# Performance work log

Measured on AMD Instinct MI355X. Metric: run time of the kernel, lower is better.

The kernel has to match this reference:

```python
import jax, jax.numpy as jnp
import numpy as np


def setup_inputs() -> dict:
    key = jax.random.key(0)
    k1, k2, k3, k4 = jax.random.split(key, 4)
    B, T, S, D = 256, 16, 32, 768
    return {
        "video_global": jax.random.normal(k1, (B, D), dtype=jnp.float32),
        "text_global": jax.random.normal(k2, (B, D), dtype=jnp.float32),
        "video_local": jax.random.normal(k3, (B, T, D), dtype=jnp.float32),
        "text_local": jax.random.normal(k4, (B, S, D), dtype=jnp.float32),
        "temp": jnp.zeros((1,), dtype=jnp.float32),  # log(1.0)
    }


def reference(video_global, text_global, video_local, text_local, temp):
    B = video_global.shape[0]
    logit_scale = jnp.exp(temp)[0]

    # ---- global contrastive loss ----
    global_sim = logit_scale * (video_global @ text_global.T)  # [B, B]
    diag = jnp.arange(B)
    loss_v2t = -jax.nn.log_softmax(global_sim, axis=1)[diag, diag].mean()
    loss_t2v = -jax.nn.log_softmax(global_sim, axis=0)[diag, diag].mean()
    loss_global = 0.5 * (loss_v2t + loss_t2v)

    # ---- local positive scores ----
    # paired (diagonal) local similarity: [B, T, S]
    sim_pos = logit_scale * jnp.einsum("btd,bsd->bts", video_local, text_local)
    time_weights = jax.nn.softmax(sim_pos.max(axis=-1), axis=-1)  # [B, T]
    pos_scores = (sim_pos.mean(axis=-1) * time_weights).sum(axis=1)  # [B]

    # ---- local negative scores (batched pairwise contraction) ----
    # [B, B, T, S]: video i vs text j, replacing the B*(B-1) tiny einsum loop
    sim_all = logit_scale * jnp.einsum("btd,csd->bcts", video_local, text_local)
    neg_full = (time_weights[:, None, :] * sim_all.mean(axis=-1)).sum(axis=-1)  # [B, B]

    # drop diagonal (i == j), preserving row-major loop order
    rows, cols = np.nonzero(~np.eye(B, dtype=bool))
    neg_scores = neg_full[rows, cols].reshape(B, B - 1)

    logits = jnp.concatenate([pos_scores[:, None], neg_scores], axis=-1)  # [B, B]
    loss_local = -jax.nn.log_softmax(logits, axis=-1)[:, 0].mean()

    return 0.6 * loss_global + 0.4 * loss_local
```

## Files before the change

### kernel.cpp

```cpp
#include <hip/hip_runtime.h>
#include <cmath>

#define BB 256
#define TT 16
#define SS 32
#define DD 768
#define LROW 260

__global__ __launch_bounds__(512) void hl_stage1(
    const float* __restrict__ vl, const float* __restrict__ tl,
    const float* __restrict__ temp,
    float* __restrict__ vw_ws, float* __restrict__ tb_ws)
{
    __shared__ float smem[12480];
    __shared__ float simb[512];
    __shared__ float rmax[16];
    __shared__ float twb[16];

    const int i   = blockIdx.x;
    const int tid = threadIdx.x;
    const float lsc = expf(temp[0]);

    const int slice = tid & 15;
    const int g     = tid >> 4;
    const int tg    = g >> 3;
    const int sg    = g & 7;

    const float* vli = vl + (size_t)i * TT * DD;
    const float* tli = tl + (size_t)i * SS * DD;

    float acc[4][4];
#pragma unroll
    for (int a = 0; a < 4; ++a)
#pragma unroll
        for (int b = 0; b < 4; ++b) acc[a][b] = 0.f;

    for (int c = 0; c < 3; ++c) {
        const int d0 = c << 8;
#pragma unroll
        for (int k = 0; k < 2; ++k) {
            int f4 = tid + (k << 9);
            int r  = f4 >> 6;
            int dc = (f4 & 63) << 2;
            *(float4*)&smem[r * LROW + dc] = *(const float4*)&vli[r * DD + d0 + dc];
        }
#pragma unroll
        for (int k = 0; k < 4; ++k) {
            int f4 = tid + (k << 9);
            int r  = f4 >> 6;
            int dc = (f4 & 63) << 2;
            *(float4*)&smem[(16 + r) * LROW + dc] = *(const float4*)&tli[r * DD + d0 + dc];
        }
        __syncthreads();
#pragma unroll
        for (int step = 0; step < 4; ++step) {
            const int db = (slice << 4) + (step << 2);
            float4 av[4], bv[4];
#pragma unroll
            for (int ti = 0; ti < 4; ++ti)
                av[ti] = *(const float4*)&smem[(tg * 4 + ti) * LROW + db];
#pragma unroll
            for (int sj = 0; sj < 4; ++sj)
                bv[sj] = *(const float4*)&smem[(16 + sg * 4 + sj) * LROW + db];
#pragma unroll
            for (int ti = 0; ti < 4; ++ti)
#pragma unroll
                for (int sj = 0; sj < 4; ++sj)
                    acc[ti][sj] += av[ti].x * bv[sj].x + av[ti].y * bv[sj].y
                                 + av[ti].z * bv[sj].z + av[ti].w * bv[sj].w;
        }
        __syncthreads();
    }

#pragma unroll
    for (int ti = 0; ti < 4; ++ti)
#pragma unroll
        for (int sj = 0; sj < 4; ++sj) {
            int t = tg * 4 + ti, s = sg * 4 + sj;
            smem[(t * 32 + s) * 17 + slice] = acc[ti][sj];
        }
    __syncthreads();
    {
        float ssum = 0.f;
#pragma unroll
        for (int k = 0; k < 16; ++k) ssum += smem[tid * 17 + k];
        simb[tid] = lsc * ssum;
    }
    __syncthreads();
    if (tid < 16) {
        float m = -3.0e38f;
        for (int s = 0; s < 32; ++s)
            m = fmaxf(m, simb[tid * 32 + ((s + tid) & 31)]);
        rmax[tid] = m;
    }
    __syncthreads();
    if (tid == 0) {
        float M = -3.0e38f;
        for (int t = 0; t < 16; ++t) M = fmaxf(M, rmax[t]);
        float ssum = 0.f;
        for (int t = 0; t < 16; ++t) {
            float e = expf(rmax[t] - M);
            twb[t] = e;
            ssum += e;
        }
        float inv = 1.0f / ssum;
        for (int t = 0; t < 16; ++t) twb[t] *= inv;
    }
    __syncthreads();

    for (int d = tid; d < DD; d += 512) {
        float vwv = 0.f;
#pragma unroll
        for (int t = 0; t < 16; ++t) vwv += twb[t] * vli[t * DD + d];
        vw_ws[(size_t)i * DD + d] = vwv;
        float tbv = 0.f;
#pragma unroll
        for (int s = 0; s < 32; ++s) tbv += tli[s * DD + d];
        tb_ws[(size_t)i * DD + d] = tbv * (1.0f / 32.0f);
    }
}

__global__ __launch_bounds__(256) void hl_gemm(
    const float* __restrict__ vg, const float* __restrict__ tg,
    const float* __restrict__ vw, const float* __restrict__ tb,
    const float* __restrict__ temp, float* __restrict__ cparts)
{
    __shared__ float As[16][68];
    __shared__ float Bs[16][68];
    __shared__ float Tb[64][68];

    const int b   = blockIdx.x;
    const int p   = b & 7;
    const int tj  = (b >> 3) & 3;
    const int ti  = (b >> 5) & 3;
    const int mat = b >> 7;
    const int tid = threadIdx.x;
    const float lsc = expf(temp[0]);

    const float* A  = mat ? vw : vg;
    const float* Bm = mat ? tb : tg;
    const int i0 = ti * 64, j0 = tj * 64, kb0 = p * 96;

    const int srow = tid >> 2, skq = tid & 3;
    const int tr = tid >> 4, tc = tid & 15;

    float acc[4][4];
#pragma unroll
    for (int r = 0; r < 4; ++r)
#pragma unroll
        for (int cc = 0; cc < 4; ++cc) acc[r][cc] = 0.f;

    for (int ch = 0; ch < 6; ++ch) {
        const int kb = kb0 + ch * 16;
        float4 a4 = *(const float4*)&A [(size_t)(i0 + srow) * DD + kb + skq * 4];
        float4 b4 = *(const float4*)&Bm[(size_t)(j0 + srow) * DD + kb + skq * 4];
        __syncthreads();
        As[skq * 4 + 0][srow] = a4.x; As[skq * 4 + 1][srow] = a4.y;
        As[skq * 4 + 2][srow] = a4.z; As[skq * 4 + 3][srow] = a4.w;
        Bs[skq * 4 + 0][srow] = b4.x; Bs[skq * 4 + 1][srow] = b4.y;
        Bs[skq * 4 + 2][srow] = b4.z; Bs[skq * 4 + 3][srow] = b4.w;
        __syncthreads();
#pragma unroll
        for (int k = 0; k < 16; ++k) {
            float4 av = *(const float4*)&As[k][tr * 4];
            float4 bv = *(const float4*)&Bs[k][tc * 4];
            float ar[4] = {av.x, av.y, av.z, av.w};
            float br[4] = {bv.x, bv.y, bv.z, bv.w};
#pragma unroll
            for (int r = 0; r < 4; ++r)
#pragma unroll
                for (int cc = 0; cc < 4; ++cc)
                    acc[r][cc] += ar[r] * br[cc];
        }
    }

    const int cm = mat ? 0 : 1;
    float* Cp = cparts + ((size_t)p * 3 + cm) * 65536;
#pragma unroll
    for (int r = 0; r < 4; ++r) {
        float4 v = {acc[r][0] * lsc, acc[r][1] * lsc, acc[r][2] * lsc, acc[r][3] * lsc};
        *(float4*)&Cp[(size_t)(i0 + tr * 4 + r) * 256 + j0 + tc * 4] = v;
    }
    if (mat == 0) {
        __syncthreads();
#pragma unroll
        for (int r = 0; r < 4; ++r)
#pragma unroll
            for (int cc = 0; cc < 4; ++cc)
                Tb[tc * 4 + cc][tr * 4 + r] = acc[r][cc] * lsc;
        __syncthreads();
        float* Ct = cparts + ((size_t)p * 3 + 2) * 65536;
#pragma unroll
        for (int r = 0; r < 4; ++r) {
            float4 v = *(const float4*)&Tb[tr * 4 + r][tc * 4];
            *(float4*)&Ct[(size_t)(j0 + tr * 4 + r) * 256 + i0 + tc * 4] = v;
        }
    }
}

__global__ __launch_bounds__(256) void hl_lse(
    const float* __restrict__ cparts, float* __restrict__ out)
{
    __shared__ float xs[256];
    __shared__ float wred[4];
    __shared__ float bcast;

    const int b   = blockIdx.x;
    const int cm  = b >> 8;
    const int row = b & 255;
    const int tid = threadIdx.x;

    float x = 0.f;
#pragma unroll
    for (int p = 0; p < 8; ++p)
        x += cparts[((size_t)p * 3 + cm) * 65536 + (size_t)row * 256 + tid];
    xs[tid] = x;

    float m = x;
#pragma unroll
    for (int off = 32; off > 0; off >>= 1)
        m = fmaxf(m, __shfl_down(m, off, 64));
    if ((tid & 63) == 0) wred[tid >> 6] = m;
    __syncthreads();
    if (tid == 0)
        bcast = fmaxf(fmaxf(wred[0], wred[1]), fmaxf(wred[2], wred[3]));
    __syncthreads();
    float M = bcast;
    float e = expf(x - M);
#pragma unroll
    for (int off = 32; off > 0; off >>= 1)
        e += __shfl_down(e, off, 64);
    if ((tid & 63) == 0) wred[tid >> 6] = e;
    __syncthreads();
    if (tid == 0) {
        float Stot = wred[0] + wred[1] + wred[2] + wred[3];
        float lse  = M + logf(Stot);
        float w    = (cm == 0) ? (0.4f / 256.0f) : (0.3f / 256.0f);
        atomicAdd(out, w * (lse - xs[row]));
    }
}

extern "C" void kernel_launch(void* const* d_in, const int* in_sizes, int n_in,
                              void* d_out, int out_size, void* d_ws, size_t ws_size,
                              hipStream_t stream)
{
    const float* vg   = (const float*)d_in[0];
    const float* tg   = (const float*)d_in[1];
    const float* vl   = (const float*)d_in[2];
    const float* tl   = (const float*)d_in[3];
    const float* temp = (const float*)d_in[4];
    float* out = (float*)d_out;

    float* vw     = (float*)d_ws;
    float* tb     = vw + (size_t)BB * DD;
    float* cparts = tb + (size_t)BB * DD;

    hipMemsetAsync(out, 0, sizeof(float) * out_size, stream);
    hl_stage1<<<dim3(BB),  dim3(512), 0, stream>>>(vl, tl, temp, vw, tb);
    hl_gemm  <<<dim3(256), dim3(256), 0, stream>>>(vg, tg, vw, tb, temp, cparts);
    hl_lse   <<<dim3(768), dim3(256), 0, stream>>>(cparts, out);
}
```

Before: 116.7 us.

## Overlap global GEMM with stage1, fuse LSE into GEMM launches, drop memset

Moves the global video-text GEMM into the first kernel as extra blocks, so it runs alongside the per-batch local similarity work. The global row/column log-sum-exp reductions now run inside the second kernel next to the local GEMM, and the local LSE moves to a small third kernel using one wave per row. The output is zeroed in-kernel instead of by a memset. Register prefetch double-buffering is added to the staged loads. This removes a separate memset and serialized phases, at the cost of heavier blocks: half the threads sit idle in the GEMM blocks, and the zeroing of out inside block 0 relies on it finishing before any atomicAdd in later kernels.

```diff
diff --git a/kernel.cpp b/kernel.cpp
--- a/kernel.cpp
+++ b/kernel.cpp
@@ -7,237 +7,330 @@
 #define DD 768
 #define LROW 260
 
-__global__ __launch_bounds__(512) void hl_stage1(
+__device__ __forceinline__ void wave_lse(
+    const float* __restrict__ cparts, float* __restrict__ out,
+    int cm, int row, float w)
+{
+    const int lane = threadIdx.x & 63;
+    float4 x = make_float4(0.f, 0.f, 0.f, 0.f);
+    const float* base = cparts + (size_t)cm * 65536 + (size_t)row * 256 + (lane << 2);
+#pragma unroll
+    for (int p = 0; p < 8; ++p) {
+        float4 v = *(const float4*)(base + (size_t)p * 3 * 65536);
+        x.x += v.x; x.y += v.y; x.z += v.z; x.w += v.w;
+    }
+    float m = fmaxf(fmaxf(x.x, x.y), fmaxf(x.z, x.w));
+#pragma unroll
+    for (int off = 32; off > 0; off >>= 1)
+        m = fmaxf(m, __shfl_xor(m, off, 64));
+    float e = expf(x.x - m) + expf(x.y - m) + expf(x.z - m) + expf(x.w - m);
+#pragma unroll
+    for (int off = 32; off > 0; off >>= 1)
+        e += __shfl_xor(e, off, 64);
+    if (lane == (row >> 2)) {
+        float lse = m + logf(e);
+        float xd = (row & 2) ? ((row & 1) ? x.w : x.z)
+                             : ((row & 1) ? x.y : x.x);
+        atomicAdd(out, w * (lse - xd));
+    }
+}
+
+__global__ __launch_bounds__(512, 4) void hl_k1(
     const float* __restrict__ vl, const float* __restrict__ tl,
+    const float* __restrict__ vgp, const float* __restrict__ tgp,
     const float* __restrict__ temp,
-    float* __restrict__ vw_ws, float* __restrict__ tb_ws)
-{
-    __shared__ float smem[12480];
-    __shared__ float simb[512];
-    __shared__ float rmax[16];
-    __shared__ float twb[16];
-
-    const int i   = blockIdx.x;
+    float* __restrict__ vw_ws, float* __restrict__ tb_ws,
+    float* __restrict__ cparts, float* __restrict__ out, int out_n)
+{
+    __shared__ float lds[13024];
     const int tid = threadIdx.x;
     const float lsc = expf(temp[0]);
 
-    const int slice = tid & 15;
-    const int g     = tid >> 4;
-    const int tg    = g >> 3;
-    const int sg    = g & 7;
-
-    const float* vli = vl + (size_t)i * TT * DD;
-    const float* tli = tl + (size_t)i * SS * DD;
-
-    float acc[4][4];
-#pragma unroll
-    for (int a = 0; a < 4; ++a)
-#pragma unroll
-        for (int b = 0; b < 4; ++b) acc[a][b] = 0.f;
-
-    for (int c = 0; c < 3; ++c) {
-        const int d0 = c << 8;
+    if (blockIdx.x < BB) {
+        float* smem  = lds;
+        float* simb  = lds + 12480;
+        float* rmaxb = lds + 12992;
+        float* twb   = lds + 13008;
+        const int i = blockIdx.x;
+        if (i == 0) {
+            for (int o = tid; o < out_n; o += 512) out[o] = 0.f;
+        }
+
+        const int slice = tid & 15;
+        const int g     = tid >> 4;
+        const int tgr   = g >> 3;
+        const int sg    = g & 7;
+
+        const float* vli = vl + (size_t)i * TT * DD;
+        const float* tli = tl + (size_t)i * SS * DD;
+
+        float acc[4][4];
+#pragma unroll
+        for (int a = 0; a < 4; ++a)
+#pragma unroll
+            for (int b = 0; b < 4; ++b) acc[a][b] = 0.f;
+
+        float4 pre[6];
 #pragma unroll
         for (int k = 0; k < 2; ++k) {
             int f4 = tid + (k << 9);
-            int r  = f4 >> 6;
-            int dc = (f4 & 63) << 2;
-            *(float4*)&smem[r * LROW + dc] = *(const float4*)&vli[r * DD + d0 + dc];
+            pre[k] = *(const float4*)&vli[(f4 >> 6) * DD + ((f4 & 63) << 2)];
         }
 #pragma unroll
         for (int k = 0; k < 4; ++k) {
             int f4 = tid + (k << 9);
-            int r  = f4 >> 6;
-            int dc = (f4 & 63) << 2;
-            *(float4*)&smem[(16 + r) * LROW + dc] = *(const float4*)&tli[r * DD + d0 + dc];
-        }
-        __syncthreads();
-#pragma unroll
-        for (int step = 0; step < 4; ++step) {
-            const int db = (slice << 4) + (step << 2);
-            float4 av[4], bv[4];
-#pragma unroll
-            for (int ti = 0; ti < 4; ++ti)
-                av[ti] = *(const float4*)&smem[(tg * 4 + ti) * LROW + db];
-#pragma unroll
-            for (int sj = 0; sj < 4; ++sj)
-                bv[sj] = *(const float4*)&smem[(16 + sg * 4 + sj) * LROW + db];
-#pragma unroll
-            for (int ti = 0; ti < 4; ++ti)
+            pre[2 + k] = *(const float4*)&tli[(f4 >> 6) * DD + ((f4 & 63) << 2)];
+        }
+
+        for (int c = 0; c < 3; ++c) {
+            __syncthreads();
+#pragma unroll
+            for (int k = 0; k < 2; ++k) {
+                int f4 = tid + (k << 9);
+                *(float4*)&smem[(f4 >> 6) * LROW + ((f4 & 63) << 2)] = pre[k];
+            }
+#pragma unroll
+            for (int k = 0; k < 4; ++k) {
+                int f4 = tid + (k << 9);
+                *(float4*)&smem[(16 + (f4 >> 6)) * LROW + ((f4 & 63) << 2)] = pre[2 + k];
+            }
+            __syncthreads();
+            if (c < 2) {
+                const int d0n = (c + 1) << 8;
+#pragma unroll
+                for (int k = 0; k < 2; ++k) {
+                    int f4 = tid + (k << 9);
+                    pre[k] = *(const float4*)&vli[(f4 >> 6) * DD + d0n + ((f4 & 63) << 2)];
+                }
+#pragma unroll
+                for (int k = 0; k < 4; ++k) {
+                    int f4 = tid + (k << 9);
+                    pre[2 + k] = *(const float4*)&tli[(f4 >> 6) * DD + d0n + ((f4 & 63) << 2)];
+                }
+            }
+#pragma unroll
+            for (int step = 0; step < 4; ++step) {
+                const int db = (slice << 4) + (step << 2);
+                float4 av[4], bv[4];
+#pragma unroll
+                for (int ti = 0; ti < 4; ++ti)
+                    av[ti] = *(const float4*)&smem[(tgr * 4 + ti) * LROW + db];
 #pragma unroll
                 for (int sj = 0; sj < 4; ++sj)
-                    acc[ti][sj] += av[ti].x * bv[sj].x + av[ti].y * bv[sj].y
-                                 + av[ti].z * bv[sj].z + av[ti].w * bv[sj].w;
-        }
-        __syncthreads();
+                    bv[sj] = *(const float4*)&smem[(16 + sg * 4 + sj) * LROW + db];
+#pragma unroll
+                for (int ti = 0; ti < 4; ++ti)
+#pragma unroll
+                    for (int sj = 0; sj < 4; ++sj)
+                        acc[ti][sj] += av[ti].x * bv[sj].x + av[ti].y * bv[sj].y
+                                     + av[ti].z * bv[sj].z + av[ti].w * bv[sj].w;
+            }
+        }
+        __syncthreads();
+
+#pragma unroll
+        for (int ti = 0; ti < 4; ++ti)
+#pragma unroll
+            for (int sj = 0; sj < 4; ++sj) {
+                int t = tgr * 4 + ti, s = sg * 4 + sj;
+                smem[(t * 32 + s) * 17 + slice] = acc[ti][sj];
+            }
+        __syncthreads();
+        {
+            float ssum = 0.f;
+#pragma unroll
+            for (int k = 0; k < 16; ++k) ssum += smem[tid * 17 + k];
+            simb[tid] = lsc * ssum;
+        }
+        __syncthreads();
+        if (tid < 16) {
+            float m = -3.0e38f;
+            for (int s = 0; s < 32; ++s)
+                m = fmaxf(m, simb[tid * 32 + ((s + tid) & 31)]);
+            rmaxb[tid] = m;
+        }
+        __syncthreads();
+        if (tid == 0) {
+            float M = -3.0e38f;
+            for (int t = 0; t < 16; ++t) M = fmaxf(M, rmaxb[t]);
+            float ssum = 0.f;
+            for (int t = 0; t < 16; ++t) {
+                float e = expf(rmaxb[t] - M);
+                twb[t] = e;
+                ssum += e;
+            }
+            float inv = 1.0f / ssum;
+            for (int t = 0; t < 16; ++t) twb[t] *= inv;
+        }
+        __syncthreads();
+
+        for (int d = tid; d < DD; d += 512) {
+            float vwv = 0.f;
+#pragma unroll
+            for (int t = 0; t < 16; ++t) vwv += twb[t] * vli[t * DD + d];
+            vw_ws[(size_t)i * DD + d] = vwv;
+            float tbv = 0.f;
+#pragma unroll
+            for (int s = 0; s < 32; ++s) tbv += tli[s * DD + d];
+            tb_ws[(size_t)i * DD + d] = tbv * (1.0f / 32.0f);
+        }
+    } else {
+        float (*As)[68] = (float (*)[68])lds;
+        float (*Bs)[68] = (float (*)[68])(lds + 1088);
+        float (*Tb)[68] = (float (*)[68])(lds + 2176);
+        const int b  = blockIdx.x - BB;
+        const int p  = b & 7;
+        const int tj = (b >> 3) & 3;
+        const int ti = b >> 5;
+        const int i0 = ti * 64, j0 = tj * 64, kb0 = p * 96;
+        const bool act = tid < 256;
+        const int srow = tid >> 2, skq = tid & 3;
+        const int tr = tid >> 4, tc = tid & 15;
+
+        float acc[4][4];
+#pragma unroll
+        for (int r = 0; r < 4; ++r)
+#pragma unroll
+            for (int cc = 0; cc < 4; ++cc) acc[r][cc] = 0.f;
+
+        float4 a4 = make_float4(0.f, 0.f, 0.f, 0.f), b4 = a4;
+        float4 a4n = a4, b4n = b4;
+        if (act) {
+            a4 = *(const float4*)&vgp[(size_t)(i0 + srow) * DD + kb0 + skq * 4];
+            b4 = *(const float4*)&tgp[(size_t)(j0 + srow) * DD + kb0 + skq * 4];
+        }
+        for (int ch = 0; ch < 6; ++ch) {
+            __syncthreads();
+            if (act) {
+                As[skq * 4 + 0][srow] = a4.x; As[skq * 4 + 1][srow] = a4.y;
+                As[skq * 4 + 2][srow] = a4.z; As[skq * 4 + 3][srow] = a4.w;
+                Bs[skq * 4 + 0][srow] = b4.x; Bs[skq * 4 + 1][srow] = b4.y;
+                Bs[skq * 4 + 2][srow] = b4.z; Bs[skq * 4 + 3][srow] = b4.w;
+            }
+            __syncthreads();
+            if (act && ch < 5) {
+                const int kb = kb0 + (ch + 1) * 16;
+                a4n = *(const float4*)&vgp[(size_t)(i0 + srow) * DD + kb + skq * 4];
+                b4n = *(const float4*)&tgp[(size_t)(j0 + srow) * DD + kb + skq * 4];
+            }
+            if (act) {
+#pragma unroll
+                for (int k = 0; k < 16; ++k) {
+                    float4 av = *(const float4*)&As[k][tr * 4];
+                    float4 bv = *(const float4*)&Bs[k][tc * 4];
+                    float ar[4] = {av.x, av.y, av.z, av.w};
+                    float br[4] = {bv.x, bv.y, bv.z, bv.w};
+#pragma unroll
+                    for (int r = 0; r < 4; ++r)
+#pragma unroll
+                        for (int cc = 0; cc < 4; ++cc)
+                            acc[r][cc] += ar[r] * br[cc];
+                }
+            }
+            a4 = a4n; b4 = b4n;
+        }
+
+        if (act) {
+            float* Cp = cparts + ((size_t)p * 3 + 1) * 65536;
+#pragma unroll
+            for (int r = 0; r < 4; ++r) {
+                float4 v = {acc[r][0] * lsc, acc[r][1] * lsc,
+                            acc[r][2] * lsc, acc[r][3] * lsc};
+                *(float4*)&Cp[(size_t)(i0 + tr * 4 + r) * 256 + j0 + tc * 4] = v;
+            }
+        }
+        __syncthreads();
+        if (act) {
+#pragma unroll
+            for (int r = 0; r < 4; ++r)
+#pragma unroll
+                for (int cc = 0; cc < 4; ++cc)
+                    Tb[tc * 4 + cc][tr * 4 + r] = acc[r][cc] * lsc;
+        }
+        __syncthreads();
+        if (act) {
+            float* Ct = cparts + ((size_t)p * 3 + 2) * 65536;
+#pragma unroll
+            for (int r = 0; r < 4; ++r) {
+                float4 v = *(const float4*)&Tb[tr * 4 + r][tc * 4];
+                *(float4*)&Ct[(size_t)(j0 + tr * 4 + r) * 256 + i0 + tc * 4] = v;
+            }
+        }
     }
-
-#pragma unroll
-    for (int ti = 0; ti < 4; ++ti)
-#pragma unroll
-        for (int sj = 0; sj < 4; ++sj) {
-            int t = tg * 4 + ti, s = sg * 4 + sj;
-            smem[(t * 32 + s) * 17 + slice] = acc[ti][sj];
-        }
-    __syncthreads();
-    {
-        float ssum = 0.f;
-#pragma unroll
-        for (int k = 0; k < 16; ++k) ssum += smem[tid * 17 + k];
-        simb[tid] = lsc * ssum;
+}
+
+__global__ __launch_bounds__(256) void hl_k2(
+    const float* __restrict__ vw, const float* __restrict__ tbm,
+    const float* __restrict__ temp, float* __restrict__ cparts,
+    float* __restrict__ out)
+{
+    const int tid = threadIdx.x;
+    const int b   = blockIdx.x;
+    if (b < 128) {
+        __shared__ float As[16][68];
+        __shared__ float Bs[16][68];
+        const float lsc = expf(temp[0]);
+        const int p = b & 7, tj = (b >> 3) & 3, ti = b >> 5;
+        const int i0 = ti * 64, j0 = tj * 64, kb0 = p * 96;
+        const int srow = tid >> 2, skq = tid & 3;
+        const int tr = tid >> 4, tc = tid & 15;
+
+        float acc[4][4];
+#pragma unroll
+        for (int r = 0; r < 4; ++r)
+#pragma unroll
+            for (int cc = 0; cc < 4; ++cc) acc[r][cc] = 0.f;
+
+        float4 a4 = *(const float4*)&vw [(size_t)(i0 + srow) * DD + kb0 + skq * 4];
+        float4 b4 = *(const float4*)&tbm[(size_t)(j0 + srow) * DD + kb0 + skq * 4];
+        float4 a4n = a4, b4n = b4;
+        for (int ch = 0; ch < 6; ++ch) {
+            __syncthreads();
+            As[skq * 4 + 0][srow] = a4.x; As[skq * 4 + 1][srow] = a4.y;
+            As[skq * 4 + 2][srow] = a4.z; As[skq * 4 + 3][srow] = a4.w;
+            Bs[skq * 4 + 0][srow] = b4.x; Bs[skq * 4 + 1][srow] = b4.y;
+            Bs[skq * 4 + 2][srow] = b4.z; Bs[skq * 4 + 3][srow] = b4.w;
+            __syncthreads();
+            if (ch < 5) {
+                const int kb = kb0 + (ch + 1) * 16;
+                a4n = *(const float4*)&vw [(size_t)(i0 + srow) * DD + kb + skq * 4];
+                b4n = *(const float4*)&tbm[(size_t)(j0 + srow) * DD + kb + skq * 4];
+            }
+#pragma unroll
+            for (int k = 0; k < 16; ++k) {
+                float4 av = *(const float4*)&As[k][tr * 4];
+                float4 bv = *(const float4*)&Bs[k][tc * 4];
+                float ar[4] = {av.x, av.y, av.z, av.w};
+                float br[4] = {bv.x, bv.y, bv.z, bv.w};
+#pragma unroll
+                for (int r = 0; r < 4; ++r)
+#pragma unroll
+                    for (int cc = 0; cc < 4; ++cc)
+                        acc[r][cc] += ar[r] * br[cc];
+            }
+            a4 = a4n; b4 = b4n;
+        }
+
+        float* Cp = cparts + (size_t)p * 3 * 65536;
+#pragma unroll
+        for (int r = 0; r < 4; ++r) {
+            float4 v = {acc[r][0] * lsc, acc[r][1] * lsc,
+                        acc[r][2] * lsc, acc[r][3] * lsc};
+            *(float4*)&Cp[(size_t)(i0 + tr * 4 + r) * 256 + j0 + tc * 4] = v;
+        }
+    } else {
+        const int idx = b - 128;
+        const int cm  = 1 + (idx >> 6);
+        const int row = ((idx & 63) << 2) + (tid >> 6);
+        wave_lse(cparts, out, cm, row, 0.3f / 256.0f);
     }
-    __syncthreads();
-    if (tid < 16) {
-        float m = -3.0e38f;
-        for (int s = 0; s < 32; ++s)
-            m = fmaxf(m, simb[tid * 32 + ((s + tid) & 31)]);
-        rmax[tid] = m;
-    }
-    __syncthreads();
-    if (tid == 0) {
-        float M = -3.0e38f;
-        for (int t = 0; t < 16; ++t) M = fmaxf(M, rmax[t]);
-        float ssum = 0.f;
-        for (int t = 0; t < 16; ++t) {
-            float e = expf(rmax[t] - M);
-            twb[t] = e;
-            ssum += e;
-        }
-        float inv = 1.0f / ssum;
-        for (int t = 0; t < 16; ++t) twb[t] *= inv;
-    }
-    __syncthreads();
-
-    for (int d = tid; d < DD; d += 512) {
-        float vwv = 0.f;
-#pragma unroll
-        for (int t = 0; t < 16; ++t) vwv += twb[t] * vli[t * DD + d];
-        vw_ws[(size_t)i * DD + d] = vwv;
-        float tbv = 0.f;
-#pragma unroll
-        for (int s = 0; s < 32; ++s) tbv += tli[s * DD + d];
-        tb_ws[(size_t)i * DD + d] = tbv * (1.0f / 32.0f);
-    }
-}
-
-__global__ __launch_bounds__(256) void hl_gemm(
-    const float* __restrict__ vg, const float* __restrict__ tg,
-    const float* __restrict__ vw, const float* __restrict__ tb,
-    const float* __restrict__ temp, float* __restrict__ cparts)
-{
-    __shared__ float As[16][68];
-    __shared__ float Bs[16][68];
-    __shared__ float Tb[64][68];
-
-    const int b   = blockIdx.x;
-    const int p   = b & 7;
-    const int tj  = (b >> 3) & 3;
-    const int ti  = (b >> 5) & 3;
-    const int mat = b >> 7;
-    const int tid = threadIdx.x;
-    const float lsc = expf(temp[0]);
-
-    const float* A  = mat ? vw : vg;
-    const float* Bm = mat ? tb : tg;
-    const int i0 = ti * 64, j0 = tj * 64, kb0 = p * 96;
-
-    const int srow = tid >> 2, skq = tid & 3;
-    const int tr = tid >> 4, tc = tid & 15;
-
-    float acc[4][4];
-#pragma unroll
-    for (int r = 0; r < 4; ++r)
-#pragma unroll
-        for (int cc = 0; cc < 4; ++cc) acc[r][cc] = 0.f;
-
-    for (int ch = 0; ch < 6; ++ch) {
-        const int kb = kb0 + ch * 16;
-        float4 a4 = *(const float4*)&A [(size_t)(i0 + srow) * DD + kb + skq * 4];
-        float4 b4 = *(const float4*)&Bm[(size_t)(j0 + srow) * DD + kb + skq * 4];
-        __syncthreads();
-        As[skq * 4 + 0][srow] = a4.x; As[skq * 4 + 1][srow] = a4.y;
-        As[skq * 4 + 2][srow] = a4.z; As[skq * 4 + 3][srow] = a4.w;
-        Bs[skq * 4 + 0][srow] = b4.x; Bs[skq * 4 + 1][srow] = b4.y;
-        Bs[skq * 4 + 2][srow] = b4.z; Bs[skq * 4 + 3][srow] = b4.w;
-        __syncthreads();
-#pragma unroll
-        for (int k = 0; k < 16; ++k) {
-            float4 av = *(const float4*)&As[k][tr * 4];
-            float4 bv = *(const float4*)&Bs[k][tc * 4];
-            float ar[4] = {av.x, av.y, av.z, av.w};
-            float br[4] = {bv.x, bv.y, bv.z, bv.w};
-#pragma unroll
-            for (int r = 0; r < 4; ++r)
-#pragma unroll
-                for (int cc = 0; cc < 4; ++cc)
-                    acc[r][cc] += ar[r] * br[cc];
-        }
-    }
-
-    const int cm = mat ? 0 : 1;
-    float* Cp = cparts + ((size_t)p * 3 + cm) * 65536;
-#pragma unroll
-    for (int r = 0; r < 4; ++r) {
-        float4 v = {acc[r][0] * lsc, acc[r][1] * lsc, acc[r][2] * lsc, acc[r][3] * lsc};
-        *(float4*)&Cp[(size_t)(i0 + tr * 4 + r) * 256 + j0 + tc * 4] = v;
-    }
-    if (mat == 0) {
-        __syncthreads();
-#pragma unroll
-        for (int r = 0; r < 4; ++r)
-#pragma unroll
-            for (int cc = 0; cc < 4; ++cc)
-                Tb[tc * 4 + cc][tr * 4 + r] = acc[r][cc] * lsc;
-        __syncthreads();
-        float* Ct = cparts + ((size_t)p * 3 + 2) * 65536;
-#pragma unroll
-        for (int r = 0; r < 4; ++r) {
-            float4 v = *(const float4*)&Tb[tr * 4 + r][tc * 4];
-            *(float4*)&Ct[(size_t)(j0 + tr * 4 + r) * 256 + i0 + tc * 4] = v;
-        }
-    }
-}
-
-__global__ __launch_bounds__(256) void hl_lse(
+}
+
+__global__ __launch_bounds__(256) void hl_k3(
     const float* __restrict__ cparts, float* __restrict__ out)
 {
-    __shared__ float xs[256];
-    __shared__ float wred[4];
-    __shared__ float bcast;
-
-    const int b   = blockIdx.x;
-    const int cm  = b >> 8;
-    const int row = b & 255;
-    const int tid = threadIdx.x;
-
-    float x = 0.f;
-#pragma unroll
-    for (int p = 0; p < 8; ++p)
-        x += cparts[((size_t)p * 3 + cm) * 65536 + (size_t)row * 256 + tid];
-    xs[tid] = x;
-
-    float m = x;
-#pragma unroll
-    for (int off = 32; off > 0; off >>= 1)
-        m = fmaxf(m, __shfl_down(m, off, 64));
-    if ((tid & 63) == 0) wred[tid >> 6] = m;
-    __syncthreads();
-    if (tid == 0)
-        bcast = fmaxf(fmaxf(wred[0], wred[1]), fmaxf(wred[2], wred[3]));
-    __syncthreads();
-    float M = bcast;
-    float e = expf(x - M);
-#pragma unroll
-    for (int off = 32; off > 0; off >>= 1)
-        e += __shfl_down(e, off, 64);
-    if ((tid & 63) == 0) wred[tid >> 6] = e;
-    __syncthreads();
-    if (tid == 0) {
-        float Stot = wred[0] + wred[1] + wred[2] + wred[3];
-        float lse  = M + logf(Stot);
-        float w    = (cm == 0) ? (0.4f / 256.0f) : (0.3f / 256.0f);
-        atomicAdd(out, w * (lse - xs[row]));
-    }
+    const int row = (blockIdx.x << 2) + (threadIdx.x >> 6);
+    wave_lse(cparts, out, 0, row, 0.4f / 256.0f);
 }
 
 extern "C" void kernel_launch(void* const* d_in, const int* in_sizes, int n_in,
@@ -252,11 +345,11 @@
     float* out = (float*)d_out;
 
     float* vw     = (float*)d_ws;
-    float* tb     = vw + (size_t)BB * DD;
-    float* cparts = tb + (size_t)BB * DD;
-
-    hipMemsetAsync(out, 0, sizeof(float) * out_size, stream);
-    hl_stage1<<<dim3(BB),  dim3(512), 0, stream>>>(vl, tl, temp, vw, tb);
-    hl_gemm  <<<dim3(256), dim3(256), 0, stream>>>(vg, tg, vw, tb, temp, cparts);
-    hl_lse   <<<dim3(768), dim3(256), 0, stream>>>(cparts, out);
-}
+    float* tbw    = vw + (size_t)BB * DD;
+    float* cparts = tbw + (size_t)BB * DD;
+
+    hl_k1<<<dim3(BB + 128), dim3(512), 0, stream>>>(vl, tl, vg, tg, temp,
+                                                    vw, tbw, cparts, out, out_size);
+    hl_k2<<<dim3(256), dim3(256), 0, stream>>>(vw, tbw, temp, cparts, out);
+    hl_k3<<<dim3(64),  dim3(256), 0, stream>>>(cparts, out);
+}
```

After: 123.2 us. +5.5%, slower.
